# Kernel tuning notes

Measured on AMD Instinct MI355X. Metric: run time of the kernel, lower is better.

## Reference

```python
import jax, jax.numpy as jnp
import numpy as np

N_NODES = 100000
N_EDGES = 1600000
D = 64


def setup_inputs() -> dict:
    key = jax.random.key(0)
    ks = jax.random.split(key, 7)
    x = jax.random.normal(ks[0], (N_NODES, D), dtype=jnp.float32)
    row = jax.random.randint(ks[1], (N_EDGES,), 0, N_NODES, dtype=jnp.int64)
    col = jax.random.randint(ks[2], (N_EDGES,), 0, N_NODES, dtype=jnp.int64)
    batch = jnp.zeros((N_NODES,), dtype=jnp.int64)
    # positive normalizer (e.g. degree-based); keep away from zero
    adj_norm = jax.random.uniform(ks[3], (N_NODES, 1), dtype=jnp.float32, minval=0.5, maxval=1.5)
    root_W = jax.random.normal(ks[4], (D, D), dtype=jnp.float32) / jnp.sqrt(D)
    root_b = jax.random.normal(ks[5], (D,), dtype=jnp.float32) * 0.01
    rel_W = jax.random.normal(ks[6], (D, D), dtype=jnp.float32) / jnp.sqrt(D)
    return {"x": x, "row": row, "col": col, "batch": batch, "adj_norm": adj_norm,
            "root_W": root_W, "root_b": root_b, "rel_W": rel_W}


def reference(x, row, col, batch, adj_norm, root_W, root_b, rel_W):
    # gather source features per edge, scatter-sum into destination nodes
    agg = jax.ops.segment_sum(x[row], col, num_segments=x.shape[0])  # [N, D]
    agg = agg / adj_norm
    rel = agg @ rel_W.T                      # Linear(bias=False)
    root = x @ root_W.T + root_b             # Linear(bias=True)
    return jax.nn.relu(rel + root)
```

## Files before the change

### kernel.cpp

```cpp
#include <hip/hip_runtime.h>

#define N_NODES 100000
#define N_EDGES 1600000
#define D 64
#define ROWW 128
#define SLOTN 64
#define NB1 196
#define BNODES 512
#define CAP 96
#define CHUNK1 8192
#define NBLK1 196

typedef __attribute__((ext_vector_type(8))) short bf16x8;
typedef __attribute__((ext_vector_type(4))) float f32x4;

__device__ __forceinline__ unsigned short f2bf(float f) {
    unsigned bits = __float_as_uint(f);
    bits += 0x7FFF + ((bits >> 16) & 1);
    return (unsigned short)(bits >> 16);
}

__global__ __launch_bounds__(1024) void part1(
    const float* __restrict__ x, const float* __restrict__ rel_W,
    const float* __restrict__ root_W, const int* __restrict__ row,
    const int* __restrict__ col,
    unsigned short* __restrict__ ab, unsigned short* __restrict__ Wb,
    int* __restrict__ cntMat, unsigned* __restrict__ edgesF)
{
    __shared__ unsigned eL[NB1 * CAP];
    __shared__ int cntL[NB1];
    const int tid = threadIdx.x;
    const int blk = blockIdx.x;

    for (int k = tid; k < NB1; k += 1024) cntL[k] = 0;
    __syncthreads();

    const int base = blk * CHUNK1;
    #pragma unroll
    for (int it = 0; it < CHUNK1 / 1024; ++it) {
        int e = base + it * 1024 + tid;
        if (e < N_EDGES) {
            int d = col[e];
            int bk = d >> 9;
            int r = atomicAdd(&cntL[bk], 1);
            if (r < CAP) eL[bk * CAP + r] = ((unsigned)(d & 511) << 17) | (unsigned)row[e];
        }
    }
    __syncthreads();

    for (int k = tid; k < NB1; k += 1024)
        cntMat[blk * NB1 + k] = min(cntL[k], CAP);

    const int wv = tid >> 6, lane = tid & 63;
    for (int bk = wv; bk < NB1; bk += 16) {
        int c = min(cntL[bk], CAP);
        unsigned* dst = edgesF + ((size_t)blk * NB1 + bk) * CAP;
        for (int i = lane; i < c; i += 64) dst[i] = eL[bk * CAP + i];
    }

    const int gt = blk * 1024 + tid;
    for (int t = gt; t < N_NODES * 8; t += NBLK1 * 1024) {
        int nrow = t >> 3, g = t & 7;
        const float4* xf = (const float4*)(x + (size_t)nrow * D + g * 8);
        float4 a = xf[0], b = xf[1];
        unsigned short u[8];
        u[0] = f2bf(a.x); u[1] = f2bf(a.y); u[2] = f2bf(a.z); u[3] = f2bf(a.w);
        u[4] = f2bf(b.x); u[5] = f2bf(b.y); u[6] = f2bf(b.z); u[7] = f2bf(b.w);
        *reinterpret_cast<uint4*>(ab + (size_t)nrow * ROWW + 64 + g * 8) =
            *reinterpret_cast<const uint4*>(u);
    }
    if (gt < 1024) {
        int j = gt >> 4, g = gt & 15;
        const float* src = (g < 8) ? (rel_W + j * 64 + g * 8) : (root_W + j * 64 + (g - 8) * 8);
        unsigned short u[8];
        #pragma unroll
        for (int i = 0; i < 8; ++i) u[i] = f2bf(src[i]);
        *reinterpret_cast<uint4*>(Wb + j * ROWW + g * 8) = *reinterpret_cast<const uint4*>(u);
    }
}

__global__ __launch_bounds__(1024) void part2(const unsigned* __restrict__ edgesF,
                                              const int* __restrict__ cntMat,
                                              int* __restrict__ deg,
                                              int* __restrict__ edge_src)
{
    __shared__ int cnt[BNODES];
    const int tid = threadIdx.x;
    const int b = blockIdx.x;
    for (int k = tid; k < BNODES; k += 1024) cnt[k] = 0;
    __syncthreads();

    const int wv = tid >> 6, lane = tid & 63;
    const int nb = b * BNODES;
    for (int sb = wv; sb < NBLK1; sb += 16) {
        int c = cntMat[sb * NB1 + b];
        const unsigned* src = edgesF + ((size_t)sb * NB1 + b) * CAP;
        for (int i = lane; i < c; i += 64) {
            unsigned e = src[i];
            int dl = e >> 17;
            int r = atomicAdd(&cnt[dl], 1);
            if (r < SLOTN) edge_src[(size_t)(nb + dl) * SLOTN + r] = (int)(e & 0x1FFFF);
        }
    }
    __syncthreads();

    for (int k = tid; k < BNODES; k += 1024) {
        int gn = nb + k;
        if (gn < N_NODES) deg[gn] = cnt[k];
    }
}

__global__ __launch_bounds__(256) void agg_kernel(unsigned short* __restrict__ ab,
                                                  const int* __restrict__ edge_src,
                                                  const int* __restrict__ deg,
                                                  const float* __restrict__ adj_norm) {
    int w = (blockIdx.x * 256 + threadIdx.x) >> 6;
    if (w >= N_NODES) return;
    int lane = threadIdx.x & 63;
    int q = lane >> 4, sub = lane & 15;
    int s = w * SLOTN;
    int dg = deg[w]; if (dg > SLOTN) dg = SLOTN;
    const unsigned short* __restrict__ xh = ab + 64 + sub * 4;

    float a0 = 0.f, a1 = 0.f, a2 = 0.f, a3 = 0.f;
    int idx = (lane < dg) ? edge_src[s + lane] : 0;

    int eb = 0;
    for (; eb + 16 <= dg; eb += 16) {
        int i0 = __shfl(idx, eb + q);
        int i1 = __shfl(idx, eb + q + 4);
        int i2 = __shfl(idx, eb + q + 8);
        int i3 = __shfl(idx, eb + q + 12);
        uint2 u0 = *reinterpret_cast<const uint2*>(xh + (size_t)i0 * ROWW);
        uint2 u1 = *reinterpret_cast<const uint2*>(xh + (size_t)i1 * ROWW);
        uint2 u2 = *reinterpret_cast<const uint2*>(xh + (size_t)i2 * ROWW);
        uint2 u3 = *reinterpret_cast<const uint2*>(xh + (size_t)i3 * ROWW);
        a0 += __uint_as_float(u0.x << 16) + __uint_as_float(u1.x << 16)
            + __uint_as_float(u2.x << 16) + __uint_as_float(u3.x << 16);
        a1 += __uint_as_float(u0.x & 0xffff0000u) + __uint_as_float(u1.x & 0xffff0000u)
            + __uint_as_float(u2.x & 0xffff0000u) + __uint_as_float(u3.x & 0xffff0000u);
        a2 += __uint_as_float(u0.y << 16) + __uint_as_float(u1.y << 16)
            + __uint_as_float(u2.y << 16) + __uint_as_float(u3.y << 16);
        a3 += __uint_as_float(u0.y & 0xffff0000u) + __uint_as_float(u1.y & 0xffff0000u)
            + __uint_as_float(u2.y & 0xffff0000u) + __uint_as_float(u3.y & 0xffff0000u);
    }
    if (eb < dg) {
        int nst = (dg - eb + 3) >> 2;
        for (int t = 0; t < nst; ++t) {
            int e = eb + q + t * 4;
            int ii = __shfl(idx, e & 63);
            uint2 u = *reinterpret_cast<const uint2*>(xh + (size_t)ii * ROWW);
            if (e < dg) {
                a0 += __uint_as_float(u.x << 16);
                a1 += __uint_as_float(u.x & 0xffff0000u);
                a2 += __uint_as_float(u.y << 16);
                a3 += __uint_as_float(u.y & 0xffff0000u);
            }
        }
    }

    a0 += __shfl_xor(a0, 16, 64); a0 += __shfl_xor(a0, 32, 64);
    a1 += __shfl_xor(a1, 16, 64); a1 += __shfl_xor(a1, 32, 64);
    a2 += __shfl_xor(a2, 16, 64); a2 += __shfl_xor(a2, 32, 64);
    a3 += __shfl_xor(a3, 16, 64); a3 += __shfl_xor(a3, 32, 64);

    if (q == 0) {
        float inv = 1.0f / adj_norm[w];
        uint2 p;
        p.x = (unsigned)f2bf(a0 * inv) | ((unsigned)f2bf(a1 * inv) << 16);
        p.y = (unsigned)f2bf(a2 * inv) | ((unsigned)f2bf(a3 * inv) << 16);
        *reinterpret_cast<uint2*>(ab + (size_t)w * ROWW + sub * 4) = p;
    }
}

#define APAD 136
__global__ __launch_bounds__(256) void fused_out_kernel(
    const unsigned short* __restrict__ ab, const unsigned short* __restrict__ Wb,
    const float* __restrict__ root_b, float* __restrict__ out)
{
    __shared__ unsigned short a_sh[64 * APAD];
    __shared__ unsigned short b_sh[64 * APAD];
    const int tid = threadIdx.x;
    const int n0 = blockIdx.x * 64;

    {
        int r = tid >> 2, seg = tid & 3;
        int gn = n0 + r;
        uint4 v0 = {0,0,0,0}, v1 = {0,0,0,0}, v2 = {0,0,0,0}, v3 = {0,0,0,0};
        if (gn < N_NODES) {
            const uint4* src = (const uint4*)(ab + (size_t)gn * ROWW + seg * 32);
            v0 = src[0]; v1 = src[1]; v2 = src[2]; v3 = src[3];
        }
        uint4* dst = (uint4*)(a_sh + r * APAD + seg * 32);
        dst[0] = v0; dst[1] = v1; dst[2] = v2; dst[3] = v3;
    }
    {
        int r = tid >> 2, seg = tid & 3;
        const uint4* src = (const uint4*)(Wb + r * ROWW + seg * 32);
        uint4* dst = (uint4*)(b_sh + r * APAD + seg * 32);
        dst[0] = src[0]; dst[1] = src[1]; dst[2] = src[2]; dst[3] = src[3];
    }
    __syncthreads();

    const int wv = tid >> 6, lane = tid & 63;
    const int quad = lane >> 4, l15 = lane & 15;

    bf16x8 afrag[4];
    const int abase = (wv * 16 + l15) * APAD + quad * 8;
    #pragma unroll
    for (int kk = 0; kk < 4; ++kk)
        afrag[kk] = *reinterpret_cast<const bf16x8*>(a_sh + abase + kk * 32);

    f32x4 acc[4] = {};
    #pragma unroll
    for (int t = 0; t < 4; ++t) {
        const int bbase = (t * 16 + l15) * APAD + quad * 8;
        #pragma unroll
        for (int kk = 0; kk < 4; ++kk) {
            bf16x8 bfrag = *reinterpret_cast<const bf16x8*>(b_sh + bbase + kk * 32);
            acc[t] = __builtin_amdgcn_mfma_f32_16x16x32_bf16(afrag[kk], bfrag, acc[t], 0, 0, 0);
        }
    }

    #pragma unroll
    for (int t = 0; t < 4; ++t) {
        int j = t * 16 + l15;
        float bias = root_b[j];
        #pragma unroll
        for (int r = 0; r < 4; ++r) {
            int node = n0 + wv * 16 + quad * 4 + r;
            if (node < N_NODES) {
                float v = acc[t][r] + bias;
                out[(size_t)node * D + j] = fmaxf(v, 0.0f);
            }
        }
    }
}

extern "C" void kernel_launch(void* const* d_in, const int* in_sizes, int n_in,
                              void* d_out, int out_size, void* d_ws, size_t ws_size,
                              hipStream_t stream)
{
    const float* x        = (const float*)d_in[0];
    const int*   row      = (const int*)d_in[1];
    const int*   col      = (const int*)d_in[2];
    const float* adj_norm = (const float*)d_in[4];
    const float* root_W   = (const float*)d_in[5];
    const float* root_b   = (const float*)d_in[6];
    const float* rel_W    = (const float*)d_in[7];
    float* out = (float*)d_out;

    char* ws = (char*)d_ws;
    unsigned short* ab = (unsigned short*)ws;  ws += (size_t)N_NODES * ROWW * 2;
    unsigned short* Wb = (unsigned short*)ws;  ws += 64 * ROWW * 2;
    int* cntMat        = (int*)ws;             ws += (size_t)NBLK1 * NB1 * 4;
    int* deg           = (int*)ws;             ws += (size_t)N_NODES * 4;
    unsigned* edgesF   = (unsigned*)ws;        ws += (size_t)NBLK1 * NB1 * CAP * 4;
    int* edge_src      = (int*)ws;

    part1<<<NBLK1, 1024, 0, stream>>>(x, rel_W, root_W, row, col, ab, Wb, cntMat, edgesF);
    part2<<<NB1, 1024, 0, stream>>>(edgesF, cntMat, deg, edge_src);
    agg_kernel<<<(N_NODES * 64 + 255) / 256, 256, 0, stream>>>(ab, edge_src, deg, adj_norm);
    fused_out_kernel<<<(N_NODES + 63) / 64, 256, 0, stream>>>(ab, Wb, root_b, out);
}
```

Measured before the change: 171.1 us.

## Fuse bucket scatter and aggregation into one kernel with LDS CSR

Merges the second bucketing pass and the aggregation kernel into a single kernel. Each block builds a per-node CSR for its 512 destination nodes in shared memory using a count pass, a prefix scan and a fill pass, then aggregates gathered bf16 rows per node. This removes the global edge_src/deg round trip, one launch and the 64-slot degree cap. In exchange, only 196 blocks of 1024 threads do the gather work, which may limit parallelism and latency hiding. edgesF is also read twice, and the count matrix is stored transposed so the block's reads are contiguous.

Result: slower. 192.5 us (+12.5%).

```diff
diff --git a/kernel.cpp b/kernel.cpp
--- a/kernel.cpp
+++ b/kernel.cpp
@@ -4,12 +4,12 @@
 #define N_EDGES 1600000
 #define D 64
 #define ROWW 128
-#define SLOTN 64
 #define NB1 196
 #define BNODES 512
 #define CAP 96
 #define CHUNK1 8192
 #define NBLK1 196
+#define EL_CAP 8960
 
 typedef __attribute__((ext_vector_type(8))) short bf16x8;
 typedef __attribute__((ext_vector_type(4))) float f32x4;
@@ -25,7 +25,7 @@
     const float* __restrict__ root_W, const int* __restrict__ row,
     const int* __restrict__ col,
     unsigned short* __restrict__ ab, unsigned short* __restrict__ Wb,
-    int* __restrict__ cntMat, unsigned* __restrict__ edgesF)
+    int* __restrict__ cntMatT, unsigned* __restrict__ edgesF)
 {
     __shared__ unsigned eL[NB1 * CAP];
     __shared__ int cntL[NB1];
@@ -49,7 +49,7 @@
     __syncthreads();
 
     for (int k = tid; k < NB1; k += 1024)
-        cntMat[blk * NB1 + k] = min(cntL[k], CAP);
+        cntMatT[k * NBLK1 + blk] = min(cntL[k], CAP);
 
     const int wv = tid >> 6, lane = tid & 63;
     for (int bk = wv; bk < NB1; bk += 16) {
@@ -79,97 +79,137 @@
     }
 }
 
-__global__ __launch_bounds__(1024) void part2(const unsigned* __restrict__ edgesF,
-                                              const int* __restrict__ cntMat,
-                                              int* __restrict__ deg,
-                                              int* __restrict__ edge_src)
+__global__ __launch_bounds__(1024) void agg2(unsigned short* __restrict__ ab,
+                                             const unsigned* __restrict__ edgesF,
+                                             const int* __restrict__ cntMatT,
+                                             const float* __restrict__ adj_norm)
 {
+    __shared__ int eLs[EL_CAP];
     __shared__ int cnt[BNODES];
+    __shared__ int off[BNODES];
+    __shared__ int cur[BNODES];
+    __shared__ int ws[16];
     const int tid = threadIdx.x;
     const int b = blockIdx.x;
+    const int wv = tid >> 6, lane = tid & 63;
+
     for (int k = tid; k < BNODES; k += 1024) cnt[k] = 0;
     __syncthreads();
 
-    const int wv = tid >> 6, lane = tid & 63;
-    const int nb = b * BNODES;
     for (int sb = wv; sb < NBLK1; sb += 16) {
-        int c = cntMat[sb * NB1 + b];
+        int c = cntMatT[b * NBLK1 + sb];
+        const unsigned* src = edgesF + ((size_t)sb * NB1 + b) * CAP;
+        for (int i = lane; i < c; i += 64)
+            atomicAdd(&cnt[src[i] >> 17], 1);
+    }
+    __syncthreads();
+
+    {
+        int v = (tid < BNODES) ? cnt[tid] : 0;
+        int s = v;
+        #pragma unroll
+        for (int o = 1; o < 64; o <<= 1) {
+            int t = __shfl_up(s, o, 64);
+            if (lane >= o) s += t;
+        }
+        if (lane == 63) ws[wv] = s;
+        __syncthreads();
+        if (wv == 0 && lane < 16) {
+            int w = ws[lane];
+            #pragma unroll
+            for (int o = 1; o < 16; o <<= 1) {
+                int t = __shfl_up(w, o, 64);
+                if (lane >= o) w += t;
+            }
+            ws[lane] = w;
+        }
+        __syncthreads();
+        if (tid < BNODES) {
+            int excl = s - v + (wv ? ws[wv - 1] : 0);
+            off[tid] = excl;
+            cur[tid] = excl;
+        }
+    }
+    __syncthreads();
+
+    for (int sb = wv; sb < NBLK1; sb += 16) {
+        int c = cntMatT[b * NBLK1 + sb];
         const unsigned* src = edgesF + ((size_t)sb * NB1 + b) * CAP;
         for (int i = lane; i < c; i += 64) {
             unsigned e = src[i];
-            int dl = e >> 17;
-            int r = atomicAdd(&cnt[dl], 1);
-            if (r < SLOTN) edge_src[(size_t)(nb + dl) * SLOTN + r] = (int)(e & 0x1FFFF);
-        }
-    }
-    __syncthreads();
-
-    for (int k = tid; k < BNODES; k += 1024) {
-        int gn = nb + k;
-        if (gn < N_NODES) deg[gn] = cnt[k];
-    }
-}
-
-__global__ __launch_bounds__(256) void agg_kernel(unsigned short* __restrict__ ab,
-                                                  const int* __restrict__ edge_src,
-                                                  const int* __restrict__ deg,
-                                                  const float* __restrict__ adj_norm) {
-    int w = (blockIdx.x * 256 + threadIdx.x) >> 6;
-    if (w >= N_NODES) return;
-    int lane = threadIdx.x & 63;
-    int q = lane >> 4, sub = lane & 15;
-    int s = w * SLOTN;
-    int dg = deg[w]; if (dg > SLOTN) dg = SLOTN;
+            int r = atomicAdd(&cur[e >> 17], 1);
+            if (r < EL_CAP) eLs[r] = (int)(e & 0x1FFFF);
+        }
+    }
+    __syncthreads();
+
+    const int q = lane >> 4, sub = lane & 15;
     const unsigned short* __restrict__ xh = ab + 64 + sub * 4;
 
-    float a0 = 0.f, a1 = 0.f, a2 = 0.f, a3 = 0.f;
-    int idx = (lane < dg) ? edge_src[s + lane] : 0;
-
-    int eb = 0;
-    for (; eb + 16 <= dg; eb += 16) {
-        int i0 = __shfl(idx, eb + q);
-        int i1 = __shfl(idx, eb + q + 4);
-        int i2 = __shfl(idx, eb + q + 8);
-        int i3 = __shfl(idx, eb + q + 12);
-        uint2 u0 = *reinterpret_cast<const uint2*>(xh + (size_t)i0 * ROWW);
-        uint2 u1 = *reinterpret_cast<const uint2*>(xh + (size_t)i1 * ROWW);
-        uint2 u2 = *reinterpret_cast<const uint2*>(xh + (size_t)i2 * ROWW);
-        uint2 u3 = *reinterpret_cast<const uint2*>(xh + (size_t)i3 * ROWW);
-        a0 += __uint_as_float(u0.x << 16) + __uint_as_float(u1.x << 16)
-            + __uint_as_float(u2.x << 16) + __uint_as_float(u3.x << 16);
-        a1 += __uint_as_float(u0.x & 0xffff0000u) + __uint_as_float(u1.x & 0xffff0000u)
-            + __uint_as_float(u2.x & 0xffff0000u) + __uint_as_float(u3.x & 0xffff0000u);
-        a2 += __uint_as_float(u0.y << 16) + __uint_as_float(u1.y << 16)
-            + __uint_as_float(u2.y << 16) + __uint_as_float(u3.y << 16);
-        a3 += __uint_as_float(u0.y & 0xffff0000u) + __uint_as_float(u1.y & 0xffff0000u)
-            + __uint_as_float(u2.y & 0xffff0000u) + __uint_as_float(u3.y & 0xffff0000u);
-    }
-    if (eb < dg) {
-        int nst = (dg - eb + 3) >> 2;
-        for (int t = 0; t < nst; ++t) {
-            int e = eb + q + t * 4;
-            int ii = __shfl(idx, e & 63);
-            uint2 u = *reinterpret_cast<const uint2*>(xh + (size_t)ii * ROWW);
-            if (e < dg) {
-                a0 += __uint_as_float(u.x << 16);
-                a1 += __uint_as_float(u.x & 0xffff0000u);
-                a2 += __uint_as_float(u.y << 16);
-                a3 += __uint_as_float(u.y & 0xffff0000u);
+    for (int t = 0; t < 32; ++t) {
+        const int dl = wv * 32 + t;
+        const int gn = b * BNODES + dl;
+        if (gn >= N_NODES) break;
+        const int o = off[dl];
+        int dg = cnt[dl];
+        if (o + dg > EL_CAP) dg = (o < EL_CAP) ? (EL_CAP - o) : 0;
+
+        float a0 = 0.f, a1 = 0.f, a2 = 0.f, a3 = 0.f;
+        int base = 0;
+        int idx = (lane < dg) ? eLs[o + lane] : 0;
+
+        while (true) {
+            int lim = dg - base; if (lim > 64) lim = 64;
+            int eb = 0;
+            for (; eb + 16 <= lim; eb += 16) {
+                int i0 = __shfl(idx, eb + q);
+                int i1 = __shfl(idx, eb + q + 4);
+                int i2 = __shfl(idx, eb + q + 8);
+                int i3 = __shfl(idx, eb + q + 12);
+                uint2 u0 = *reinterpret_cast<const uint2*>(xh + (size_t)i0 * ROWW);
+                uint2 u1 = *reinterpret_cast<const uint2*>(xh + (size_t)i1 * ROWW);
+                uint2 u2 = *reinterpret_cast<const uint2*>(xh + (size_t)i2 * ROWW);
+                uint2 u3 = *reinterpret_cast<const uint2*>(xh + (size_t)i3 * ROWW);
+                a0 += __uint_as_float(u0.x << 16) + __uint_as_float(u1.x << 16)
+                    + __uint_as_float(u2.x << 16) + __uint_as_float(u3.x << 16);
+                a1 += __uint_as_float(u0.x & 0xffff0000u) + __uint_as_float(u1.x & 0xffff0000u)
+                    + __uint_as_float(u2.x & 0xffff0000u) + __uint_as_float(u3.x & 0xffff0000u);
+                a2 += __uint_as_float(u0.y << 16) + __uint_as_float(u1.y << 16)
+                    + __uint_as_float(u2.y << 16) + __uint_as_float(u3.y << 16);
+                a3 += __uint_as_float(u0.y & 0xffff0000u) + __uint_as_float(u1.y & 0xffff0000u)
+                    + __uint_as_float(u2.y & 0xffff0000u) + __uint_as_float(u3.y & 0xffff0000u);
             }
-        }
-    }
-
-    a0 += __shfl_xor(a0, 16, 64); a0 += __shfl_xor(a0, 32, 64);
-    a1 += __shfl_xor(a1, 16, 64); a1 += __shfl_xor(a1, 32, 64);
-    a2 += __shfl_xor(a2, 16, 64); a2 += __shfl_xor(a2, 32, 64);
-    a3 += __shfl_xor(a3, 16, 64); a3 += __shfl_xor(a3, 32, 64);
-
-    if (q == 0) {
-        float inv = 1.0f / adj_norm[w];
-        uint2 p;
-        p.x = (unsigned)f2bf(a0 * inv) | ((unsigned)f2bf(a1 * inv) << 16);
-        p.y = (unsigned)f2bf(a2 * inv) | ((unsigned)f2bf(a3 * inv) << 16);
-        *reinterpret_cast<uint2*>(ab + (size_t)w * ROWW + sub * 4) = p;
+            if (eb < lim) {
+                int nst = (lim - eb + 3) >> 2;
+                for (int tt = 0; tt < nst; ++tt) {
+                    int e = eb + q + tt * 4;
+                    int ii = __shfl(idx, e & 63);
+                    uint2 u = *reinterpret_cast<const uint2*>(xh + (size_t)ii * ROWW);
+                    if (e < lim) {
+                        a0 += __uint_as_float(u.x << 16);
+                        a1 += __uint_as_float(u.x & 0xffff0000u);
+                        a2 += __uint_as_float(u.y << 16);
+                        a3 += __uint_as_float(u.y & 0xffff0000u);
+                    }
+                }
+            }
+            base += 64;
+            if (base >= dg) break;
+            idx = (base + lane < dg) ? eLs[o + base + lane] : 0;
+        }
+
+        a0 += __shfl_xor(a0, 16, 64); a0 += __shfl_xor(a0, 32, 64);
+        a1 += __shfl_xor(a1, 16, 64); a1 += __shfl_xor(a1, 32, 64);
+        a2 += __shfl_xor(a2, 16, 64); a2 += __shfl_xor(a2, 32, 64);
+        a3 += __shfl_xor(a3, 16, 64); a3 += __shfl_xor(a3, 32, 64);
+
+        if (q == 0) {
+            float inv = 1.0f / adj_norm[gn];
+            uint2 p;
+            p.x = (unsigned)f2bf(a0 * inv) | ((unsigned)f2bf(a1 * inv) << 16);
+            p.y = (unsigned)f2bf(a2 * inv) | ((unsigned)f2bf(a3 * inv) << 16);
+            *reinterpret_cast<uint2*>(ab + (size_t)gn * ROWW + sub * 4) = p;
+        }
     }
 }
 
@@ -253,13 +293,10 @@
     char* ws = (char*)d_ws;
     unsigned short* ab = (unsigned short*)ws;  ws += (size_t)N_NODES * ROWW * 2;
     unsigned short* Wb = (unsigned short*)ws;  ws += 64 * ROWW * 2;
-    int* cntMat        = (int*)ws;             ws += (size_t)NBLK1 * NB1 * 4;
-    int* deg           = (int*)ws;             ws += (size_t)N_NODES * 4;
-    unsigned* edgesF   = (unsigned*)ws;        ws += (size_t)NBLK1 * NB1 * CAP * 4;
-    int* edge_src      = (int*)ws;
-
-    part1<<<NBLK1, 1024, 0, stream>>>(x, rel_W, root_W, row, col, ab, Wb, cntMat, edgesF);
-    part2<<<NB1, 1024, 0, stream>>>(edgesF, cntMat, deg, edge_src);
-    agg_kernel<<<(N_NODES * 64 + 255) / 256, 256, 0, stream>>>(ab, edge_src, deg, adj_norm);
+    int* cntMatT       = (int*)ws;             ws += (size_t)NBLK1 * NB1 * 4;
+    unsigned* edgesF   = (unsigned*)ws;
+
+    part1<<<NBLK1, 1024, 0, stream>>>(x, rel_W, root_W, row, col, ab, Wb, cntMatT, edgesF);
+    agg2<<<NB1, 1024, 0, stream>>>(ab, edgesF, cntMatT, adj_norm);
     fused_out_kernel<<<(N_NODES + 63) / 64, 256, 0, stream>>>(ab, Wb, root_b, out);
 }
```

## Fuse edge bucketing, aggregation and GEMM into one kernel using LDS edge lists

Applied to the files above, without the earlier changes.

Replaces the second bucketing kernel, the aggregation kernel and the output GEMM kernel with a single kernel. Each block filters its slice of a 512-node bucket, builds per-node edge lists in shared memory, aggregates neighbor features into shared memory, and feeds them directly to MFMA alongside x. This removes intermediate global buffers (edge_src, deg, aggregated rows) and two launches, and shrinks the x buffer stride. In exchange, each bucket's edge data is re-read by eight blocks and weight fragments come from global memory instead of LDS.

Result: slower. 239.9 us (+40.2%).

```diff
diff --git a/kernel.cpp b/kernel.cpp
--- a/kernel.cpp
+++ b/kernel.cpp
@@ -3,13 +3,14 @@
 #define N_NODES 100000
 #define N_EDGES 1600000
 #define D 64
-#define ROWW 128
-#define SLOTN 64
+#define XROW 64
+#define WROW 128
 #define NB1 196
-#define BNODES 512
 #define CAP 96
 #define CHUNK1 8192
 #define NBLK1 196
+#define SLOTN 64
+#define ASH 72
 
 typedef __attribute__((ext_vector_type(8))) short bf16x8;
 typedef __attribute__((ext_vector_type(4))) float f32x4;
@@ -25,7 +26,7 @@
     const float* __restrict__ root_W, const int* __restrict__ row,
     const int* __restrict__ col,
     unsigned short* __restrict__ ab, unsigned short* __restrict__ Wb,
-    int* __restrict__ cntMat, unsigned* __restrict__ edgesF)
+    int* __restrict__ cntMatT, unsigned* __restrict__ edgesF)
 {
     __shared__ unsigned eL[NB1 * CAP];
     __shared__ int cntL[NB1];
@@ -49,7 +50,7 @@
     __syncthreads();
 
     for (int k = tid; k < NB1; k += 1024)
-        cntMat[blk * NB1 + k] = min(cntL[k], CAP);
+        cntMatT[k * NBLK1 + blk] = min(cntL[k], CAP);
 
     const int wv = tid >> 6, lane = tid & 63;
     for (int bk = wv; bk < NB1; bk += 16) {
@@ -66,7 +67,7 @@
         unsigned short u[8];
         u[0] = f2bf(a.x); u[1] = f2bf(a.y); u[2] = f2bf(a.z); u[3] = f2bf(a.w);
         u[4] = f2bf(b.x); u[5] = f2bf(b.y); u[6] = f2bf(b.z); u[7] = f2bf(b.w);
-        *reinterpret_cast<uint4*>(ab + (size_t)nrow * ROWW + 64 + g * 8) =
+        *reinterpret_cast<uint4*>(ab + (size_t)nrow * XROW + g * 8) =
             *reinterpret_cast<const uint4*>(u);
     }
     if (gt < 1024) {
@@ -75,164 +76,132 @@
         unsigned short u[8];
         #pragma unroll
         for (int i = 0; i < 8; ++i) u[i] = f2bf(src[i]);
-        *reinterpret_cast<uint4*>(Wb + j * ROWW + g * 8) = *reinterpret_cast<const uint4*>(u);
-    }
-}
-
-__global__ __launch_bounds__(1024) void part2(const unsigned* __restrict__ edgesF,
-                                              const int* __restrict__ cntMat,
-                                              int* __restrict__ deg,
-                                              int* __restrict__ edge_src)
+        *reinterpret_cast<uint4*>(Wb + j * WROW + g * 8) = *reinterpret_cast<const uint4*>(u);
+    }
+}
+
+__global__ __launch_bounds__(256, 6) void agg_gemm(
+    const unsigned short* __restrict__ ab, const unsigned* __restrict__ edgesF,
+    const int* __restrict__ cntMatT, const float* __restrict__ adj_norm,
+    const unsigned short* __restrict__ Wb, const float* __restrict__ root_b,
+    float* __restrict__ out)
 {
-    __shared__ int cnt[BNODES];
+    __shared__ int eLs[64 * SLOTN];
+    __shared__ unsigned short a_sh[64 * ASH];
+    __shared__ int cnt[64];
     const int tid = threadIdx.x;
     const int b = blockIdx.x;
-    for (int k = tid; k < BNODES; k += 1024) cnt[k] = 0;
-    __syncthreads();
-
     const int wv = tid >> 6, lane = tid & 63;
-    const int nb = b * BNODES;
-    for (int sb = wv; sb < NBLK1; sb += 16) {
-        int c = cntMat[sb * NB1 + b];
-        const unsigned* src = edgesF + ((size_t)sb * NB1 + b) * CAP;
+    const int wnd = b >> 3, e8 = b & 7;
+
+    if (tid < 64) cnt[tid] = 0;
+    __syncthreads();
+
+    for (int sb = wv; sb < NBLK1; sb += 4) {
+        int c = cntMatT[wnd * NBLK1 + sb];
+        const unsigned* src = edgesF + ((size_t)sb * NB1 + wnd) * CAP;
         for (int i = lane; i < c; i += 64) {
             unsigned e = src[i];
-            int dl = e >> 17;
-            int r = atomicAdd(&cnt[dl], 1);
-            if (r < SLOTN) edge_src[(size_t)(nb + dl) * SLOTN + r] = (int)(e & 0x1FFFF);
-        }
-    }
-    __syncthreads();
-
-    for (int k = tid; k < BNODES; k += 1024) {
-        int gn = nb + k;
-        if (gn < N_NODES) deg[gn] = cnt[k];
-    }
-}
-
-__global__ __launch_bounds__(256) void agg_kernel(unsigned short* __restrict__ ab,
-                                                  const int* __restrict__ edge_src,
-                                                  const int* __restrict__ deg,
-                                                  const float* __restrict__ adj_norm) {
-    int w = (blockIdx.x * 256 + threadIdx.x) >> 6;
-    if (w >= N_NODES) return;
-    int lane = threadIdx.x & 63;
-    int q = lane >> 4, sub = lane & 15;
-    int s = w * SLOTN;
-    int dg = deg[w]; if (dg > SLOTN) dg = SLOTN;
-    const unsigned short* __restrict__ xh = ab + 64 + sub * 4;
-
-    float a0 = 0.f, a1 = 0.f, a2 = 0.f, a3 = 0.f;
-    int idx = (lane < dg) ? edge_src[s + lane] : 0;
-
-    int eb = 0;
-    for (; eb + 16 <= dg; eb += 16) {
-        int i0 = __shfl(idx, eb + q);
-        int i1 = __shfl(idx, eb + q + 4);
-        int i2 = __shfl(idx, eb + q + 8);
-        int i3 = __shfl(idx, eb + q + 12);
-        uint2 u0 = *reinterpret_cast<const uint2*>(xh + (size_t)i0 * ROWW);
-        uint2 u1 = *reinterpret_cast<const uint2*>(xh + (size_t)i1 * ROWW);
-        uint2 u2 = *reinterpret_cast<const uint2*>(xh + (size_t)i2 * ROWW);
-        uint2 u3 = *reinterpret_cast<const uint2*>(xh + (size_t)i3 * ROWW);
-        a0 += __uint_as_float(u0.x << 16) + __uint_as_float(u1.x << 16)
-            + __uint_as_float(u2.x << 16) + __uint_as_float(u3.x << 16);
-        a1 += __uint_as_float(u0.x & 0xffff0000u) + __uint_as_float(u1.x & 0xffff0000u)
-            + __uint_as_float(u2.x & 0xffff0000u) + __uint_as_float(u3.x & 0xffff0000u);
-        a2 += __uint_as_float(u0.y << 16) + __uint_as_float(u1.y << 16)
-            + __uint_as_float(u2.y << 16) + __uint_as_float(u3.y << 16);
-        a3 += __uint_as_float(u0.y & 0xffff0000u) + __uint_as_float(u1.y & 0xffff0000u)
-            + __uint_as_float(u2.y & 0xffff0000u) + __uint_as_float(u3.y & 0xffff0000u);
-    }
-    if (eb < dg) {
-        int nst = (dg - eb + 3) >> 2;
-        for (int t = 0; t < nst; ++t) {
-            int e = eb + q + t * 4;
-            int ii = __shfl(idx, e & 63);
-            uint2 u = *reinterpret_cast<const uint2*>(xh + (size_t)ii * ROWW);
-            if (e < dg) {
-                a0 += __uint_as_float(u.x << 16);
-                a1 += __uint_as_float(u.x & 0xffff0000u);
-                a2 += __uint_as_float(u.y << 16);
-                a3 += __uint_as_float(u.y & 0xffff0000u);
+            int dl = (int)(e >> 17);
+            if ((dl >> 6) == e8) {
+                int ln = dl & 63;
+                int r = atomicAdd(&cnt[ln], 1);
+                if (r < SLOTN) eLs[ln * SLOTN + r] = (int)(e & 0x1FFFF);
             }
         }
     }
-
-    a0 += __shfl_xor(a0, 16, 64); a0 += __shfl_xor(a0, 32, 64);
-    a1 += __shfl_xor(a1, 16, 64); a1 += __shfl_xor(a1, 32, 64);
-    a2 += __shfl_xor(a2, 16, 64); a2 += __shfl_xor(a2, 32, 64);
-    a3 += __shfl_xor(a3, 16, 64); a3 += __shfl_xor(a3, 32, 64);
-
-    if (q == 0) {
-        float inv = 1.0f / adj_norm[w];
-        uint2 p;
-        p.x = (unsigned)f2bf(a0 * inv) | ((unsigned)f2bf(a1 * inv) << 16);
-        p.y = (unsigned)f2bf(a2 * inv) | ((unsigned)f2bf(a3 * inv) << 16);
-        *reinterpret_cast<uint2*>(ab + (size_t)w * ROWW + sub * 4) = p;
-    }
-}
-
-#define APAD 136
-__global__ __launch_bounds__(256) void fused_out_kernel(
-    const unsigned short* __restrict__ ab, const unsigned short* __restrict__ Wb,
-    const float* __restrict__ root_b, float* __restrict__ out)
-{
-    __shared__ unsigned short a_sh[64 * APAD];
-    __shared__ unsigned short b_sh[64 * APAD];
-    const int tid = threadIdx.x;
-    const int n0 = blockIdx.x * 64;
-
-    {
-        int r = tid >> 2, seg = tid & 3;
-        int gn = n0 + r;
-        uint4 v0 = {0,0,0,0}, v1 = {0,0,0,0}, v2 = {0,0,0,0}, v3 = {0,0,0,0};
-        if (gn < N_NODES) {
-            const uint4* src = (const uint4*)(ab + (size_t)gn * ROWW + seg * 32);
-            v0 = src[0]; v1 = src[1]; v2 = src[2]; v3 = src[3];
-        }
-        uint4* dst = (uint4*)(a_sh + r * APAD + seg * 32);
-        dst[0] = v0; dst[1] = v1; dst[2] = v2; dst[3] = v3;
-    }
-    {
-        int r = tid >> 2, seg = tid & 3;
-        const uint4* src = (const uint4*)(Wb + r * ROWW + seg * 32);
-        uint4* dst = (uint4*)(b_sh + r * APAD + seg * 32);
-        dst[0] = src[0]; dst[1] = src[1]; dst[2] = src[2]; dst[3] = src[3];
-    }
-    __syncthreads();
-
-    const int wv = tid >> 6, lane = tid & 63;
-    const int quad = lane >> 4, l15 = lane & 15;
-
+    __syncthreads();
+
+    const int q = lane >> 4, sub = lane & 15;
+    const unsigned short* __restrict__ xh = ab + sub * 4;
+
+    for (int t = 0; t < 16; ++t) {
+        const int ln = wv * 16 + t;
+        const int gn = b * 64 + ln;
+        if (gn >= N_NODES) break;
+        int dg = cnt[ln]; if (dg > SLOTN) dg = SLOTN;
+
+        float a0 = 0.f, a1 = 0.f, a2 = 0.f, a3 = 0.f;
+        int idx = (lane < dg) ? eLs[ln * SLOTN + lane] : 0;
+
+        int eb = 0;
+        for (; eb + 16 <= dg; eb += 16) {
+            int i0 = __shfl(idx, eb + q);
+            int i1 = __shfl(idx, eb + q + 4);
+            int i2 = __shfl(idx, eb + q + 8);
+            int i3 = __shfl(idx, eb + q + 12);
+            uint2 u0 = *reinterpret_cast<const uint2*>(xh + (size_t)i0 * XROW);
+            uint2 u1 = *reinterpret_cast<const uint2*>(xh + (size_t)i1 * XROW);
+            uint2 u2 = *reinterpret_cast<const uint2*>(xh + (size_t)i2 * XROW);
+            uint2 u3 = *reinterpret_cast<const uint2*>(xh + (size_t)i3 * XROW);
+            a0 += __uint_as_float(u0.x << 16) + __uint_as_float(u1.x << 16)
+                + __uint_as_float(u2.x << 16) + __uint_as_float(u3.x << 16);
+            a1 += __uint_as_float(u0.x & 0xffff0000u) + __uint_as_float(u1.x & 0xffff0000u)
+                + __uint_as_float(u2.x & 0xffff0000u) + __uint_as_float(u3.x & 0xffff0000u);
+            a2 += __uint_as_float(u0.y << 16) + __uint_as_float(u1.y << 16)
+                + __uint_as_float(u2.y << 16) + __uint_as_float(u3.y << 16);
+            a3 += __uint_as_float(u0.y & 0xffff0000u) + __uint_as_float(u1.y & 0xffff0000u)
+                + __uint_as_float(u2.y & 0xffff0000u) + __uint_as_float(u3.y & 0xffff0000u);
+        }
+        if (eb < dg) {
+            int nst = (dg - eb + 3) >> 2;
+            for (int tt = 0; tt < nst; ++tt) {
+                int e = eb + q + tt * 4;
+                int ii = __shfl(idx, e & 63);
+                uint2 u = *reinterpret_cast<const uint2*>(xh + (size_t)ii * XROW);
+                if (e < dg) {
+                    a0 += __uint_as_float(u.x << 16);
+                    a1 += __uint_as_float(u.x & 0xffff0000u);
+                    a2 += __uint_as_float(u.y << 16);
+                    a3 += __uint_as_float(u.y & 0xffff0000u);
+                }
+            }
+        }
+
+        a0 += __shfl_xor(a0, 16, 64); a0 += __shfl_xor(a0, 32, 64);
+        a1 += __shfl_xor(a1, 16, 64); a1 += __shfl_xor(a1, 32, 64);
+        a2 += __shfl_xor(a2, 16, 64); a2 += __shfl_xor(a2, 32, 64);
+        a3 += __shfl_xor(a3, 16, 64); a3 += __shfl_xor(a3, 32, 64);
+
+        if (q == 0) {
+            float inv = 1.0f / adj_norm[gn];
+            uint2 p;
+            p.x = (unsigned)f2bf(a0 * inv) | ((unsigned)f2bf(a1 * inv) << 16);
+            p.y = (unsigned)f2bf(a2 * inv) | ((unsigned)f2bf(a3 * inv) << 16);
+            *reinterpret_cast<uint2*>(a_sh + ln * ASH + sub * 4) = p;
+        }
+    }
+    __syncthreads();
+
+    const int arow = wv * 16 + sub;
+    const int gnr = b * 64 + arow;
+    const size_t gx = (size_t)((gnr < N_NODES) ? gnr : 0) * XROW;
     bf16x8 afrag[4];
-    const int abase = (wv * 16 + l15) * APAD + quad * 8;
-    #pragma unroll
-    for (int kk = 0; kk < 4; ++kk)
-        afrag[kk] = *reinterpret_cast<const bf16x8*>(a_sh + abase + kk * 32);
+    afrag[0] = *reinterpret_cast<const bf16x8*>(a_sh + arow * ASH + q * 8);
+    afrag[1] = *reinterpret_cast<const bf16x8*>(a_sh + arow * ASH + q * 8 + 32);
+    afrag[2] = *reinterpret_cast<const bf16x8*>(ab + gx + q * 8);
+    afrag[3] = *reinterpret_cast<const bf16x8*>(ab + gx + q * 8 + 32);
 
     f32x4 acc[4] = {};
     #pragma unroll
     for (int t = 0; t < 4; ++t) {
-        const int bbase = (t * 16 + l15) * APAD + quad * 8;
         #pragma unroll
         for (int kk = 0; kk < 4; ++kk) {
-            bf16x8 bfrag = *reinterpret_cast<const bf16x8*>(b_sh + bbase + kk * 32);
+            bf16x8 bfrag = *reinterpret_cast<const bf16x8*>(
+                Wb + (t * 16 + sub) * WROW + q * 8 + kk * 32);
             acc[t] = __builtin_amdgcn_mfma_f32_16x16x32_bf16(afrag[kk], bfrag, acc[t], 0, 0, 0);
         }
     }
 
     #pragma unroll
     for (int t = 0; t < 4; ++t) {
-        int j = t * 16 + l15;
+        int j = t * 16 + sub;
         float bias = root_b[j];
         #pragma unroll
         for (int r = 0; r < 4; ++r) {
-            int node = n0 + wv * 16 + quad * 4 + r;
-            if (node < N_NODES) {
-                float v = acc[t][r] + bias;
-                out[(size_t)node * D + j] = fmaxf(v, 0.0f);
-            }
+            int node = b * 64 + wv * 16 + q * 4 + r;
+            if (node < N_NODES)
+                out[(size_t)node * D + j] = fmaxf(acc[t][r] + bias, 0.0f);
         }
     }
 }
@@ -251,15 +220,11 @@
     float* out = (float*)d_out;
 
     char* ws = (char*)d_ws;
-    unsigned short* ab = (unsigned short*)ws;  ws += (size_t)N_NODES * ROWW * 2;
-    unsigned short* Wb = (unsigned short*)ws;  ws += 64 * ROWW * 2;
-    int* cntMat        = (int*)ws;             ws += (size_t)NBLK1 * NB1 * 4;
-    int* deg           = (int*)ws;             ws += (size_t)N_NODES * 4;
-    unsigned* edgesF   = (unsigned*)ws;        ws += (size_t)NBLK1 * NB1 * CAP * 4;
-    int* edge_src      = (int*)ws;
-
-    part1<<<NBLK1, 1024, 0, stream>>>(x, rel_W, root_W, row, col, ab, Wb, cntMat, edgesF);
-    part2<<<NB1, 1024, 0, stream>>>(edgesF, cntMat, deg, edge_src);
-    agg_kernel<<<(N_NODES * 64 + 255) / 256, 256, 0, stream>>>(ab, edge_src, deg, adj_norm);
-    fused_out_kernel<<<(N_NODES + 63) / 64, 256, 0, stream>>>(ab, Wb, root_b, out);
-}
+    unsigned short* ab = (unsigned short*)ws;  ws += (size_t)N_NODES * XROW * 2;
+    unsigned short* Wb = (unsigned short*)ws;  ws += 64 * WROW * 2;
+    int* cntMatT       = (int*)ws;             ws += (size_t)NBLK1 * NB1 * 4;
+    unsigned* edgesF   = (unsigned*)ws;
+
+    part1<<<NBLK1, 1024, 0, stream>>>(x, rel_W, root_W, row, col, ab, Wb, cntMatT, edgesF);
+    agg_gemm<<<NB1 * 8, 256, 0, stream>>>(ab, edgesF, cntMatT, adj_norm, Wb, root_b, out);
+}
```
